# Kernel tuning notes

Hardware: AMD Instinct MI355X
Metric: run time of the kernel (lower is better)

Reference implementation:

```python
import jax, jax.numpy as jnp
import numpy as np

C = 512          # channels
G = 32           # GroupNorm groups (flax default)
H = 8            # num_heads
EPS = 1e-6       # GroupNorm epsilon (flax default)
SPATIAL = (64, 64)


def setup_inputs() -> dict:
    key = jax.random.key(0)
    k1, k2 = jax.random.split(key)
    x = jax.random.normal(k1, SPATIAL + (C,), dtype=jnp.float32)
    gn_scale = jnp.ones((C,), dtype=jnp.float32)
    gn_bias = jnp.zeros((C,), dtype=jnp.float32)
    w_qkv = jax.random.normal(k2, (C, 3 * C), dtype=jnp.float32) / np.sqrt(C)
    b_qkv = jnp.zeros((3 * C,), dtype=jnp.float32)
    return {"x": x, "gn_scale": gn_scale, "gn_bias": gn_bias,
            "w_qkv": w_qkv, "b_qkv": b_qkv}


def reference(x, gn_scale, gn_bias, w_qkv, b_qkv):
    spatial_shape = x.shape[:-1]
    T = int(np.prod(spatial_shape))
    xf = x.reshape(T, C)

    # GroupNorm over (all spatial positions, channels within group) per group
    xg = xf.reshape(T, G, C // G)
    mean = jnp.mean(xg, axis=(0, 2), keepdims=True)
    var = jnp.var(xg, axis=(0, 2), keepdims=True)
    xn = ((xg - mean) * jax.lax.rsqrt(var + EPS)).reshape(T, C)
    xn = xn * gn_scale + gn_bias

    # QKV projection; note strided split: reshape (T, 3C) -> (T, C, 3)
    qkv = (xn @ w_qkv + b_qkv).reshape(T, C, 3)
    q, k, v = qkv[..., 0], qkv[..., 1], qkv[..., 2]

    ch = C // H
    scale = 1.0 / np.sqrt(np.sqrt(ch))
    qh = (q * scale).reshape(T, H, ch)
    kh = (k * scale).reshape(T, H, ch)
    vh = v.reshape(T, H, ch)

    w = jnp.einsum('thc,shc->ths', qh, kh)      # (T, H, T) attention scores
    w = jax.nn.softmax(w, axis=-1)
    a = jnp.einsum('ths,shc->thc', w, vh)       # (T, H, ch)
    return a.reshape(spatial_shape + (C,))
```

## Files before the change

### kernel.cpp

```cpp
#include <hip/hip_runtime.h>
#include <hip/hip_bf16.h>
#include <stdint.h>

typedef __attribute__((ext_vector_type(8))) short bf16x8;
typedef __attribute__((ext_vector_type(4))) float f32x4;
typedef unsigned short u16;
typedef unsigned int u32;

constexpr int T  = 4096;
constexpr int C  = 512;
constexpr int H  = 8;
constexpr int CH = 64;
constexpr float EPS = 1e-6f;
constexpr float QKS   = 0.35355339059327378f;
constexpr float QKS_Q = 0.35355339059327378f * 1.4426950408889634f;
constexpr float M2    = 11.541560327111707f;

__device__ __forceinline__ float bf2f(u16 u) {
    union { unsigned int i; float f; } v; v.i = ((unsigned int)u) << 16; return v.f;
}
__device__ __forceinline__ u16 f2bf(float f) {
    union { float f; unsigned int i; } v; v.f = f;
    return (u16)((v.i + 0x7FFFu + ((v.i >> 16) & 1u)) >> 16);
}
__device__ __forceinline__ u32 pk2bf(float a, float b) {
    __hip_bfloat162 h = __float22bfloat162_rn(make_float2(a, b));
    u32 r; __builtin_memcpy(&r, &h, 4); return r;
}
__device__ __forceinline__ float ldin(const void* p, int i, int f32) {
    return f32 ? ((const float*)p)[i] : bf2f(((const u16*)p)[i]);
}
__device__ __forceinline__ void async16(const void* g, void* l) {
    __builtin_amdgcn_global_load_lds(
        (const __attribute__((address_space(1))) void*)g,
        (__attribute__((address_space(3))) void*)l,
        16, 0, 0);
}

__global__ void k_stats1(const void* x, float* gs, int* flag) {
    int b = blockIdx.x, tid = threadIdx.x;
    int lane = tid & 63, w = tid >> 6;
    __shared__ int cnt;
    __shared__ float red[4][32][2];
    if (tid == 0) cnt = 0;
    __syncthreads();
    const u16* u = (const u16*)x;
    int huge = 0;
    for (int i = tid; i < 1024; i += 256) {
        float a = fabsf(bf2f(u[i]));
        if (!(a < 1e4f)) huge++;
    }
    if (huge) atomicAdd(&cnt, huge);
    __syncthreads();
    int f32 = (cnt >= 8) ? 1 : 0;
    if (tid == 0) *flag = f32;
    float s1 = 0.f, s2 = 0.f;
    if (f32) {
        const float4* xp = (const float4*)x + b * 4096;
        #pragma unroll
        for (int i = 0; i < 16; i++) {
            float4 v = xp[i * 256 + tid];
            s1 += (v.x + v.y) + (v.z + v.w);
            s2 += (v.x*v.x + v.y*v.y) + (v.z*v.z + v.w*v.w);
        }
        s1 += __shfl_xor(s1, 1); s2 += __shfl_xor(s2, 1);
        s1 += __shfl_xor(s1, 2); s2 += __shfl_xor(s2, 2);
        if ((lane & 3) == 0) {
            int gl = (lane >> 2) + 16 * (w & 1);
            red[w][gl][0] = s1; red[w][gl][1] = s2;
        }
        __syncthreads();
        if (tid < 32) {
            int g = tid, w0 = (g < 16) ? 0 : 1;
            atomicAdd(&gs[g * 2],     red[w0][g][0] + red[w0 + 2][g][0]);
            atomicAdd(&gs[g * 2 + 1], red[w0][g][1] + red[w0 + 2][g][1]);
        }
    } else {
        const uint4* xp = (const uint4*)x + b * 2048;
        #pragma unroll
        for (int i = 0; i < 8; i++) {
            uint4 v = xp[i * 256 + tid];
            float f[8] = { bf2f((u16)(v.x&0xffff)), bf2f((u16)(v.x>>16)),
                           bf2f((u16)(v.y&0xffff)), bf2f((u16)(v.y>>16)),
                           bf2f((u16)(v.z&0xffff)), bf2f((u16)(v.z>>16)),
                           bf2f((u16)(v.w&0xffff)), bf2f((u16)(v.w>>16)) };
            #pragma unroll
            for (int j = 0; j < 8; j++) { s1 += f[j]; s2 += f[j]*f[j]; }
        }
        s1 += __shfl_xor(s1, 1); s2 += __shfl_xor(s2, 1);
        if ((lane & 1) == 0) { red[w][lane >> 1][0] = s1; red[w][lane >> 1][1] = s2; }
        __syncthreads();
        if (tid < 32) {
            int g = tid;
            atomicAdd(&gs[g * 2],     red[0][g][0]+red[1][g][0]+red[2][g][0]+red[3][g][0]);
            atomicAdd(&gs[g * 2 + 1], red[0][g][1]+red[1][g][1]+red[2][g][1]+red[3][g][1]);
        }
    }
}

__global__ void k_fuse(const void* x, const float* __restrict__ gs,
                       const void* gsc, const void* gbi, const void* wq,
                       u16* __restrict__ xn, u16* __restrict__ wt,
                       const int* __restrict__ flag) {
    int bx = blockIdx.x, tid = threadIdx.x;
    int f32 = *flag;
    if (bx < 1024) {
        int idx = (bx * 256 + tid) * 8;
        int c = idx & (C - 1);
        int g = c >> 4;
        float mean = gs[2 * g] * (1.0f / 65536.0f);
        float var  = gs[2 * g + 1] * (1.0f / 65536.0f) - mean * mean;
        float rstd = rsqrtf(var + EPS);
        float v[8];
        if (f32) {
            float4 x0 = *(const float4*)((const float*)x + idx);
            float4 x1 = *(const float4*)((const float*)x + idx + 4);
            v[0]=x0.x; v[1]=x0.y; v[2]=x0.z; v[3]=x0.w;
            v[4]=x1.x; v[5]=x1.y; v[6]=x1.z; v[7]=x1.w;
        } else {
            uint4 u = *(const uint4*)((const u16*)x + idx);
            v[0]=bf2f((u16)(u.x&0xffff)); v[1]=bf2f((u16)(u.x>>16));
            v[2]=bf2f((u16)(u.y&0xffff)); v[3]=bf2f((u16)(u.y>>16));
            v[4]=bf2f((u16)(u.z&0xffff)); v[5]=bf2f((u16)(u.z>>16));
            v[6]=bf2f((u16)(u.w&0xffff)); v[7]=bf2f((u16)(u.w>>16));
        }
        float r[8];
        #pragma unroll
        for (int i = 0; i < 8; i++) {
            float a = rstd * ldin(gsc, c + i, f32);
            r[i] = v[i] * a + (ldin(gbi, c + i, f32) - mean * a);
        }
        uint4 o;
        o.x = pk2bf(r[0], r[1]); o.y = pk2bf(r[2], r[3]);
        o.z = pk2bf(r[4], r[5]); o.w = pk2bf(r[6], r[7]);
        *(uint4*)(xn + idx) = o;
    } else {
        __shared__ u16 Wl[48][64];
        int b = bx - 1024;
        int k0 = (b >> 5) * 64, c0 = (b & 31) * 48;
        #pragma unroll
        for (int it = 0; it < 3; it++) {
            int u_ = it * 256 + tid;
            int r = u_ / 12, cu = u_ % 12;
            int gi = (k0 + r) * 1536 + c0 + cu * 4;
            float v0, v1, v2, v3;
            if (f32) {
                float4 t4 = *(const float4*)((const float*)wq + gi);
                v0 = t4.x; v1 = t4.y; v2 = t4.z; v3 = t4.w;
            } else {
                uint2 t2 = *(const uint2*)((const u16*)wq + gi);
                v0 = bf2f((u16)(t2.x & 0xffff)); v1 = bf2f((u16)(t2.x >> 16));
                v2 = bf2f((u16)(t2.y & 0xffff)); v3 = bf2f((u16)(t2.y >> 16));
            }
            Wl[cu*4+0][r] = f2bf(v0); Wl[cu*4+1][r] = f2bf(v1);
            Wl[cu*4+2][r] = f2bf(v2); Wl[cu*4+3][r] = f2bf(v3);
        }
        __syncthreads();
        #pragma unroll
        for (int it = 0; it < 2; it++) {
            int u_ = it * 256 + tid;
            if (u_ < 384) {
                int mrow = u_ >> 3, kc = u_ & 7;
                int j = mrow >> 4, cci = mrow & 15;
                int m = j * 512 + (c0 / 3) + cci;
                int cl = 3 * cci + j;
                uint4 val = *(const uint4*)&Wl[cl][kc * 8];
                *(uint4*)(wt + m * 512 + k0 + kc * 8) = val;
            }
        }
    }
}

__global__ __launch_bounds__(256) void k_gemm(
    const u16* __restrict__ xn, const u16* __restrict__ wt,
    const void* __restrict__ bq, const int* __restrict__ flag,
    u16* __restrict__ qh, u16* __restrict__ kh, u16* __restrict__ vt)
{
    __shared__ u16 Al[64 * 64];
    __shared__ u16 Bl[128 * 64];
    __shared__ u16 Tt[4 * 2048];
    int bx = blockIdx.x;
    int bm = bx & 63, bn = bx >> 6;
    int tid = threadIdx.x;
    int w = tid >> 6, lane = tid & 63, quad = lane >> 4, l15 = lane & 15;
    f32x4 acc[4][2] = {};
    const u16* Ag = xn + bm * 64 * 512;
    const u16* Bg = wt + bn * 128 * 512;
    for (int k0 = 0; k0 < 512; k0 += 64) {
        __syncthreads();
        #pragma unroll
        for (int i = 0; i < 2; i++) {
            int L = i * 256 + tid, row = L >> 3, cc = ((L & 7) ^ (row & 7)) * 8;
            async16(Ag + row * 512 + k0 + cc, (void*)(Al + L * 8));
        }
        #pragma unroll
        for (int i = 0; i < 4; i++) {
            int L = i * 256 + tid, row = L >> 3, cc = ((L & 7) ^ (row & 7)) * 8;
            async16(Bg + row * 512 + k0 + cc, (void*)(Bl + L * 8));
        }
        __syncthreads();
        #pragma unroll
        for (int kk = 0; kk < 2; kk++) {
            bf16x8 af[4], bfr[2];
            #pragma unroll
            for (int mi = 0; mi < 4; mi++) {
                int row = mi * 16 + l15;
                af[mi] = *(const bf16x8*)(Al + row * 64 + (((kk * 4 + quad) ^ (row & 7)) * 8));
            }
            #pragma unroll
            for (int ni = 0; ni < 2; ni++) {
                int row = w * 32 + ni * 16 + l15;
                bfr[ni] = *(const bf16x8*)(Bl + row * 64 + (((kk * 4 + quad) ^ (row & 7)) * 8));
            }
            #pragma unroll
            for (int mi = 0; mi < 4; mi++)
                #pragma unroll
                for (int ni = 0; ni < 2; ni++)
                    acc[mi][ni] = __builtin_amdgcn_mfma_f32_16x16x32_bf16(
                        af[mi], bfr[ni], acc[mi][ni], 0, 0, 0);
        }
    }
    int f32 = *flag;
    int t_base = bm * 64;
    int j = bn >> 2;
    if (j < 2) {
        u16* dst = j ? kh : qh;
        float s = j ? QKS : QKS_Q;
        #pragma unroll
        for (int ni = 0; ni < 2; ni++) {
            int n = bn * 128 + w * 32 + ni * 16 + l15;
            int r = n & 511, hh = r >> 6, cc = r & 63;
            float bias = ldin(bq, 3 * r + j, f32);
            #pragma unroll
            for (int mi = 0; mi < 4; mi++) {
                int tq = t_base + mi * 16 + quad * 4;
                #pragma unroll
                for (int rg = 0; rg < 4; rg++)
                    dst[(hh * T + tq + rg) * CH + cc] = f2bf((acc[mi][ni][rg] + bias) * s);
            }
        }
    } else {
        u16* Tw = Tt + w * 2048;
        int rbase = (bn - 8) * 128 + w * 32;
        int hh = rbase >> 6;
        #pragma unroll
        for (int ni = 0; ni < 2; ni++) {
            int r = rbase + ni * 16 + l15;
            float bias = ldin(bq, 3 * (r & 511) + 2, f32);
            int rl = ni * 16 + l15;
            #pragma unroll
            for (int mi = 0; mi < 4; mi++) {
                uint2 pv;
                pv.x = pk2bf(acc[mi][ni][0] + bias, acc[mi][ni][1] + bias);
                pv.y = pk2bf(acc[mi][ni][2] + bias, acc[mi][ni][3] + bias);
                int cs = (mi * 2 + (quad >> 1)) ^ (rl & 7);
                *(uint2*)((u32*)Tw + rl * 32 + cs * 4 + (quad & 1) * 2) = pv;
            }
        }
        int cc_hi = (w & 1) * 32;
        #pragma unroll
        for (int rr = 0; rr < 4; rr++) {
            int rl = rr * 8 + (lane >> 3);
            int g = lane & 7;
            bf16x8 val = *(const bf16x8*)(Tw + rl * 64 + ((g ^ (rl & 7)) * 8));
            *(uint4*)(vt + (hh * CH + cc_hi + rl) * T + t_base + g * 8) = *(uint4*)&val;
        }
    }
}

__global__ __launch_bounds__(256, 4) void k_attn(
    const u16* __restrict__ qh, const u16* __restrict__ kh,
    const u16* __restrict__ vt, float* __restrict__ opart, float* __restrict__ ls)
{
    __shared__ char lds[40960];
    u16* K0 = (u16*)lds;
    u16* Vl = (u16*)(lds + 16384);
    int bx = blockIdx.x;
    int h = bx >> 7, qb = (bx >> 2) & 31, ks = bx & 3;
    int t0 = qb * 128;
    int tid = threadIdx.x;
    int w = tid >> 6, lane = tid & 63, quad = lane >> 4, l15 = lane & 15;
    u16* Pw = (u16*)(lds + 24576 + w * 4096);

    const u16* Kg = kh + (h * T + ks * 1024) * CH;
    const u16* Vg = vt + h * CH * T + ks * 1024;

    bf16x8 bq[2][2];
    #pragma unroll
    for (int ni = 0; ni < 2; ni++) {
        int t = t0 + w * 32 + ni * 16 + l15;
        #pragma unroll
        for (int kk = 0; kk < 2; kk++)
            bq[ni][kk] = *(const bf16x8*)(qh + (h * T + t) * CH + kk * 32 + quad * 8);
    }

    #pragma unroll
    for (int i = 0; i < 2; i++) {
        int L = i * 256 + tid, row = L >> 3, cc = ((L & 7) ^ (row & 7)) * 8;
        async16(Kg + row * CH + cc, (void*)(K0 + L * 8));
    }

    f32x4 o[4][2] = {};
    float lsum[2] = {0.f, 0.f};

    for (int kt = 0; kt < 16; kt++) {
        u16* Kc = K0 + (kt & 1) * 4096;
        __syncthreads();
        int s0 = kt * 64;
        #pragma unroll
        for (int i = 0; i < 2; i++) {
            int L = i * 256 + tid, row = L >> 3, cc = ((L & 7) ^ (row & 7)) * 8;
            async16(Vg + row * T + s0 + cc, (void*)(Vl + L * 8));
        }
        if (kt < 15) {
            const u16* Kn = Kg + (s0 + 64) * CH;
            u16* Kd = K0 + ((kt + 1) & 1) * 4096;
            #pragma unroll
            for (int i = 0; i < 2; i++) {
                int L = i * 256 + tid, row = L >> 3, cc = ((L & 7) ^ (row & 7)) * 8;
                async16(Kn + row * CH + cc, (void*)(Kd + L * 8));
            }
        }
        f32x4 s[4][2] = {};
        #pragma unroll
        for (int kk = 0; kk < 2; kk++)
            #pragma unroll
            for (int mi = 0; mi < 4; mi++) {
                int r = mi * 16 + l15;
                bf16x8 aK = *(const bf16x8*)(Kc + r * 64 + (((kk * 4 + quad) ^ (r & 7)) * 8));
                #pragma unroll
                for (int ni = 0; ni < 2; ni++)
                    s[mi][ni] = __builtin_amdgcn_mfma_f32_16x16x32_bf16(
                        aK, bq[ni][kk], s[mi][ni], 0, 0, 0);
            }
        #pragma unroll
        for (int ni = 0; ni < 2; ni++) {
            int rl = ni * 16 + l15;
            u32* prow = (u32*)Pw + rl * 32;
            float rs = 0.f;
            #pragma unroll
            for (int mi = 0; mi < 4; mi++) {
                float e0 = exp2f(s[mi][ni][0] - M2);
                float e1 = exp2f(s[mi][ni][1] - M2);
                float e2 = exp2f(s[mi][ni][2] - M2);
                float e3 = exp2f(s[mi][ni][3] - M2);
                rs += (e0 + e1) + (e2 + e3);
                int c2 = (mi * 2 + (quad >> 1)) ^ (rl & 7);
                uint2 pv; pv.x = pk2bf(e0, e1); pv.y = pk2bf(e2, e3);
                *(uint2*)(prow + c2 * 4 + (quad & 1) * 2) = pv;
            }
            lsum[ni] += rs;
        }
        __syncthreads();
        #pragma unroll
        for (int kk = 0; kk < 2; kk++) {
            bf16x8 bp[2];
            #pragma unroll
            for (int ni = 0; ni < 2; ni++) {
                int rl = ni * 16 + l15;
                bp[ni] = *(const bf16x8*)(Pw + rl * 64 + (((kk * 4 + quad) ^ (rl & 7)) * 8));
            }
            #pragma unroll
            for (int mi = 0; mi < 4; mi++) {
                int r = mi * 16 + l15;
                bf16x8 av = *(const bf16x8*)(Vl + r * 64 + (((kk * 4 + quad) ^ (r & 7)) * 8));
                #pragma unroll
                for (int ni = 0; ni < 2; ni++)
                    o[mi][ni] = __builtin_amdgcn_mfma_f32_16x16x32_bf16(
                        av, bp[ni], o[mi][ni], 0, 0, 0);
            }
        }
    }
    #pragma unroll
    for (int ni = 0; ni < 2; ni++) {
        lsum[ni] += __shfl_xor(lsum[ni], 16);
        lsum[ni] += __shfl_xor(lsum[ni], 32);
    }
    __syncthreads();
    float* S = (float*)(lds + w * 10240);
    #pragma unroll
    for (int ni = 0; ni < 2; ni++) {
        int rl = ni * 16 + l15;
        if (quad == 0) S[2176 + rl] = lsum[ni];
        #pragma unroll
        for (int mi = 0; mi < 4; mi++)
            #pragma unroll
            for (int rg = 0; rg < 4; rg++)
                S[rl * 68 + mi * 16 + quad * 4 + rg] = o[mi][ni][rg];
    }
    int q2 = lane >> 1, dh = (lane & 1) * 32;
    int t = t0 + w * 32 + q2;
    float* od = opart + (((ks * 8 + h) * T) + t) * 64 + dh;
    #pragma unroll
    for (int i = 0; i < 8; i++)
        *(f32x4*)(od + i * 4) = *(const f32x4*)(S + q2 * 68 + dh + i * 4);
    if (lane < 32 && (lane & 1) == 0)
        ls[(ks * 8 + h) * T + t0 + w * 32 + (lane >> 1)] = S[2176 + (lane >> 1)];
    if (lane >= 32 && (lane & 1) == 0)
        ls[(ks * 8 + h) * T + t0 + w * 32 + (lane >> 1)] = S[2176 + (lane >> 1)];
}

__global__ void k_fin(const float* __restrict__ opart, const float* __restrict__ ls,
                      void* __restrict__ out, const int* __restrict__ flag) {
    int idx = (blockIdx.x * 256 + threadIdx.x) * 8;
    int d0 = idx & 63;
    int ht = idx >> 6;
    int t = ht & (T - 1), h = ht >> 12;
    float inv = 1.0f / (ls[ht] + ls[32768 + ht] + ls[65536 + ht] + ls[98304 + ht]);
    float v[8] = {};
    #pragma unroll
    for (int ks = 0; ks < 4; ks++) {
        float4 a0 = *(const float4*)(opart + ks * 2097152 + idx);
        float4 a1 = *(const float4*)(opart + ks * 2097152 + idx + 4);
        v[0] += a0.x; v[1] += a0.y; v[2] += a0.z; v[3] += a0.w;
        v[4] += a1.x; v[5] += a1.y; v[6] += a1.z; v[7] += a1.w;
    }
    #pragma unroll
    for (int i = 0; i < 8; i++) v[i] *= inv;
    int gbase = t * C + h * CH + d0;
    if (*flag) {
        *(float4*)((float*)out + gbase)     = make_float4(v[0], v[1], v[2], v[3]);
        *(float4*)((float*)out + gbase + 4) = make_float4(v[4], v[5], v[6], v[7]);
    } else {
        uint4 o;
        o.x = pk2bf(v[0], v[1]); o.y = pk2bf(v[2], v[3]);
        o.z = pk2bf(v[4], v[5]); o.w = pk2bf(v[6], v[7]);
        *(uint4*)((u16*)out + gbase) = o;
    }
}

extern "C" void kernel_launch(void* const* d_in, const int* in_sizes, int n_in,
                              void* d_out, int out_size, void* d_ws, size_t ws_size,
                              hipStream_t stream) {
    const void* x   = d_in[0];
    const void* gsc = d_in[1];
    const void* gbi = d_in[2];
    const void* wq  = d_in[3];
    const void* bq  = d_in[4];
    char* ws = (char*)d_ws;
    int*   flag = (int*)ws;
    float* gs   = (float*)(ws + 256);
    char* base = ws + 8192;
    u16* qh = (u16*)(base);
    u16* kh = (u16*)(base + 4194304);
    u16* vt = (u16*)(base + 8388608);
    u16* xn = (u16*)(base + 12582912);
    u16* wt = (u16*)(base + 16777216);
    float* opart = (float*)(base + 12582912);
    float* ls    = (float*)(base + 46137344);

    hipMemsetAsync(gs, 0, 256, stream);
    hipLaunchKernelGGL(k_stats1, dim3(128),  dim3(256), 0, stream, x, gs, flag);
    hipLaunchKernelGGL(k_fuse,   dim3(1280), dim3(256), 0, stream, x, gs, gsc, gbi, wq, xn, wt, flag);
    hipLaunchKernelGGL(k_gemm,   dim3(768),  dim3(256), 0, stream, xn, wt, bq, flag, qh, kh, vt);
    hipLaunchKernelGGL(k_attn,   dim3(1024), dim3(256), 0, stream, qh, kh, vt, opart, ls);
    hipLaunchKernelGGL(k_fin,    dim3(1024), dim3(256), 0, stream, opart, ls, d_out, flag);
}
```

Measured before the change: 175.2 us.

## Use 32x32 MFMA in attention with register P exchange; double-buffer GEMM tiles

```diff
diff --git a/kernel.cpp b/kernel.cpp
--- a/kernel.cpp
+++ b/kernel.cpp
@@ -4,6 +4,7 @@
 
 typedef __attribute__((ext_vector_type(8))) short bf16x8;
 typedef __attribute__((ext_vector_type(4))) float f32x4;
+typedef __attribute__((ext_vector_type(16))) float f32x16;
 typedef unsigned short u16;
 typedef unsigned int u32;
 
@@ -176,9 +177,9 @@
     const void* __restrict__ bq, const int* __restrict__ flag,
     u16* __restrict__ qh, u16* __restrict__ kh, u16* __restrict__ vt)
 {
-    __shared__ u16 Al[64 * 64];
-    __shared__ u16 Bl[128 * 64];
-    __shared__ u16 Tt[4 * 2048];
+    __shared__ char smem[49152];
+    u16* Al = (u16*)smem;
+    u16* Bl = (u16*)(smem + 16384);
     int bx = blockIdx.x;
     int bm = bx & 63, bn = bx >> 6;
     int tid = threadIdx.x;
@@ -186,31 +187,49 @@
     f32x4 acc[4][2] = {};
     const u16* Ag = xn + bm * 64 * 512;
     const u16* Bg = wt + bn * 128 * 512;
-    for (int k0 = 0; k0 < 512; k0 += 64) {
-        __syncthreads();
-        #pragma unroll
-        for (int i = 0; i < 2; i++) {
-            int L = i * 256 + tid, row = L >> 3, cc = ((L & 7) ^ (row & 7)) * 8;
-            async16(Ag + row * 512 + k0 + cc, (void*)(Al + L * 8));
-        }
-        #pragma unroll
-        for (int i = 0; i < 4; i++) {
-            int L = i * 256 + tid, row = L >> 3, cc = ((L & 7) ^ (row & 7)) * 8;
-            async16(Bg + row * 512 + k0 + cc, (void*)(Bl + L * 8));
-        }
-        __syncthreads();
+
+    #pragma unroll
+    for (int i = 0; i < 2; i++) {
+        int L = i * 256 + tid, row = L >> 3, cc = ((L & 7) ^ (row & 7)) * 8;
+        async16(Ag + row * 512 + cc, (void*)(Al + L * 8));
+    }
+    #pragma unroll
+    for (int i = 0; i < 4; i++) {
+        int L = i * 256 + tid, row = L >> 3, cc = ((L & 7) ^ (row & 7)) * 8;
+        async16(Bg + row * 512 + cc, (void*)(Bl + L * 8));
+    }
+
+    #pragma unroll
+    for (int ki = 0; ki < 8; ki++) {
+        __syncthreads();
+        if (ki < 7) {
+            int kn = (ki + 1) * 64;
+            int bo = ((ki + 1) & 1);
+            #pragma unroll
+            for (int i = 0; i < 2; i++) {
+                int L = i * 256 + tid, row = L >> 3, cc = ((L & 7) ^ (row & 7)) * 8;
+                async16(Ag + row * 512 + kn + cc, (void*)(Al + bo * 4096 + L * 8));
+            }
+            #pragma unroll
+            for (int i = 0; i < 4; i++) {
+                int L = i * 256 + tid, row = L >> 3, cc = ((L & 7) ^ (row & 7)) * 8;
+                async16(Bg + row * 512 + kn + cc, (void*)(Bl + bo * 8192 + L * 8));
+            }
+        }
+        const u16* Ab = Al + (ki & 1) * 4096;
+        const u16* Bb = Bl + (ki & 1) * 8192;
         #pragma unroll
         for (int kk = 0; kk < 2; kk++) {
             bf16x8 af[4], bfr[2];
             #pragma unroll
             for (int mi = 0; mi < 4; mi++) {
                 int row = mi * 16 + l15;
-                af[mi] = *(const bf16x8*)(Al + row * 64 + (((kk * 4 + quad) ^ (row & 7)) * 8));
+                af[mi] = *(const bf16x8*)(Ab + row * 64 + (((kk * 4 + quad) ^ (row & 7)) * 8));
             }
             #pragma unroll
             for (int ni = 0; ni < 2; ni++) {
                 int row = w * 32 + ni * 16 + l15;
-                bfr[ni] = *(const bf16x8*)(Bl + row * 64 + (((kk * 4 + quad) ^ (row & 7)) * 8));
+                bfr[ni] = *(const bf16x8*)(Bb + row * 64 + (((kk * 4 + quad) ^ (row & 7)) * 8));
             }
             #pragma unroll
             for (int mi = 0; mi < 4; mi++)
@@ -240,6 +259,8 @@
             }
         }
     } else {
+        __syncthreads();
+        u16* Tt = (u16*)smem;
         u16* Tw = Tt + w * 2048;
         int rbase = (bn - 8) * 128 + w * 32;
         int hh = rbase >> 6;
@@ -272,26 +293,34 @@
     const u16* __restrict__ qh, const u16* __restrict__ kh,
     const u16* __restrict__ vt, float* __restrict__ opart, float* __restrict__ ls)
 {
-    __shared__ char lds[40960];
+    __shared__ char lds[24576];
     u16* K0 = (u16*)lds;
     u16* Vl = (u16*)(lds + 16384);
     int bx = blockIdx.x;
     int h = bx >> 7, qb = (bx >> 2) & 31, ks = bx & 3;
     int t0 = qb * 128;
     int tid = threadIdx.x;
-    int w = tid >> 6, lane = tid & 63, quad = lane >> 4, l15 = lane & 15;
-    u16* Pw = (u16*)(lds + 24576 + w * 4096);
+    int w = tid >> 6, lane = tid & 63;
+    int l31 = lane & 31, hi = lane >> 5;
 
     const u16* Kg = kh + (h * T + ks * 1024) * CH;
     const u16* Vg = vt + h * CH * T + ks * 1024;
 
-    bf16x8 bq[2][2];
-    #pragma unroll
-    for (int ni = 0; ni < 2; ni++) {
-        int t = t0 + w * 32 + ni * 16 + l15;
-        #pragma unroll
-        for (int kk = 0; kk < 2; kk++)
-            bq[ni][kk] = *(const bf16x8*)(qh + (h * T + t) * CH + kk * 32 + quad * 8);
+    int off[2][4];
+    #pragma unroll
+    for (int rt = 0; rt < 2; rt++)
+        #pragma unroll
+        for (int c = 0; c < 4; c++) {
+            int row = rt * 32 + l31;
+            off[rt][c] = row * 64 + (((2 * c + hi) ^ (row & 7)) * 8);
+        }
+
+    bf16x8 bq[4];
+    {
+        const u16* qrow = qh + (h * T + t0 + w * 32 + l31) * CH;
+        #pragma unroll
+        for (int ksi = 0; ksi < 4; ksi++)
+            bq[ksi] = *(const bf16x8*)(qrow + ksi * 16 + hi * 8);
     }
 
     #pragma unroll
@@ -300,20 +329,20 @@
         async16(Kg + row * CH + cc, (void*)(K0 + L * 8));
     }
 
-    f32x4 o[4][2] = {};
-    float lsum[2] = {0.f, 0.f};
+    f32x16 o[2] = {};
+    float lsum = 0.f;
 
     for (int kt = 0; kt < 16; kt++) {
-        u16* Kc = K0 + (kt & 1) * 4096;
-        __syncthreads();
-        int s0 = kt * 64;
+        const u16* Kc = K0 + (kt & 1) * 4096;
+        __syncthreads();
+        int kbase = kt * 64;
         #pragma unroll
         for (int i = 0; i < 2; i++) {
             int L = i * 256 + tid, row = L >> 3, cc = ((L & 7) ^ (row & 7)) * 8;
-            async16(Vg + row * T + s0 + cc, (void*)(Vl + L * 8));
+            async16(Vg + row * T + kbase + cc, (void*)(Vl + L * 8));
         }
         if (kt < 15) {
-            const u16* Kn = Kg + (s0 + 64) * CH;
+            const u16* Kn = Kg + (kbase + 64) * CH;
             u16* Kd = K0 + ((kt + 1) & 1) * 4096;
             #pragma unroll
             for (int i = 0; i < 2; i++) {
@@ -321,83 +350,69 @@
                 async16(Kn + row * CH + cc, (void*)(Kd + L * 8));
             }
         }
-        f32x4 s[4][2] = {};
-        #pragma unroll
-        for (int kk = 0; kk < 2; kk++)
-            #pragma unroll
-            for (int mi = 0; mi < 4; mi++) {
-                int r = mi * 16 + l15;
-                bf16x8 aK = *(const bf16x8*)(Kc + r * 64 + (((kk * 4 + quad) ^ (r & 7)) * 8));
-                #pragma unroll
-                for (int ni = 0; ni < 2; ni++)
-                    s[mi][ni] = __builtin_amdgcn_mfma_f32_16x16x32_bf16(
-                        aK, bq[ni][kk], s[mi][ni], 0, 0, 0);
-            }
-        #pragma unroll
-        for (int ni = 0; ni < 2; ni++) {
-            int rl = ni * 16 + l15;
-            u32* prow = (u32*)Pw + rl * 32;
+        f32x16 sa[2] = {};
+        #pragma unroll
+        for (int t = 0; t < 2; t++)
+            #pragma unroll
+            for (int ksi = 0; ksi < 4; ksi++) {
+                bf16x8 aK = *(const bf16x8*)(Kc + off[t][ksi]);
+                sa[t] = __builtin_amdgcn_mfma_f32_32x32x16_bf16(aK, bq[ksi], sa[t], 0, 0, 0);
+            }
+        u32 bp[4][4];
+        #pragma unroll
+        for (int t = 0; t < 2; t++) {
+            u32 p[8], xch[8];
             float rs = 0.f;
             #pragma unroll
-            for (int mi = 0; mi < 4; mi++) {
-                float e0 = exp2f(s[mi][ni][0] - M2);
-                float e1 = exp2f(s[mi][ni][1] - M2);
-                float e2 = exp2f(s[mi][ni][2] - M2);
-                float e3 = exp2f(s[mi][ni][3] - M2);
-                rs += (e0 + e1) + (e2 + e3);
-                int c2 = (mi * 2 + (quad >> 1)) ^ (rl & 7);
-                uint2 pv; pv.x = pk2bf(e0, e1); pv.y = pk2bf(e2, e3);
-                *(uint2*)(prow + c2 * 4 + (quad & 1) * 2) = pv;
-            }
-            lsum[ni] += rs;
-        }
-        __syncthreads();
-        #pragma unroll
-        for (int kk = 0; kk < 2; kk++) {
-            bf16x8 bp[2];
-            #pragma unroll
-            for (int ni = 0; ni < 2; ni++) {
-                int rl = ni * 16 + l15;
-                bp[ni] = *(const bf16x8*)(Pw + rl * 64 + (((kk * 4 + quad) ^ (rl & 7)) * 8));
-            }
-            #pragma unroll
-            for (int mi = 0; mi < 4; mi++) {
-                int r = mi * 16 + l15;
-                bf16x8 av = *(const bf16x8*)(Vl + r * 64 + (((kk * 4 + quad) ^ (r & 7)) * 8));
-                #pragma unroll
-                for (int ni = 0; ni < 2; ni++)
-                    o[mi][ni] = __builtin_amdgcn_mfma_f32_16x16x32_bf16(
-                        av, bp[ni], o[mi][ni], 0, 0, 0);
-            }
-        }
-    }
-    #pragma unroll
-    for (int ni = 0; ni < 2; ni++) {
-        lsum[ni] += __shfl_xor(lsum[ni], 16);
-        lsum[ni] += __shfl_xor(lsum[ni], 32);
-    }
+            for (int pi = 0; pi < 8; pi++) {
+                float e0 = exp2f(sa[t][2 * pi]     - M2);
+                float e1 = exp2f(sa[t][2 * pi + 1] - M2);
+                rs += e0 + e1;
+                p[pi] = pk2bf(e0, e1);
+            }
+            lsum += rs;
+            #pragma unroll
+            for (int pi = 0; pi < 8; pi++) xch[pi] = (u32)__shfl_xor((int)p[pi], 32);
+            #pragma unroll
+            for (int k2 = 0; k2 < 2; k2++) {
+                int kst = t * 2 + k2;
+                bp[kst][0] = hi ? xch[4*k2+2] : p[4*k2+0];
+                bp[kst][1] = hi ? xch[4*k2+3] : p[4*k2+1];
+                bp[kst][2] = hi ? p[4*k2+2]   : xch[4*k2+0];
+                bp[kst][3] = hi ? p[4*k2+3]   : xch[4*k2+1];
+            }
+        }
+        __syncthreads();
+        #pragma unroll
+        for (int dt = 0; dt < 2; dt++)
+            #pragma unroll
+            for (int kst = 0; kst < 4; kst++) {
+                bf16x8 aV = *(const bf16x8*)(Vl + off[dt][kst]);
+                bf16x8 bpv;
+                __builtin_memcpy(&bpv, bp[kst], 16);
+                o[dt] = __builtin_amdgcn_mfma_f32_32x32x16_bf16(aV, bpv, o[dt], 0, 0, 0);
+            }
+    }
+    lsum += __shfl_xor(lsum, 32);
+
     __syncthreads();
-    float* S = (float*)(lds + w * 10240);
-    #pragma unroll
-    for (int ni = 0; ni < 2; ni++) {
-        int rl = ni * 16 + l15;
-        if (quad == 0) S[2176 + rl] = lsum[ni];
-        #pragma unroll
-        for (int mi = 0; mi < 4; mi++)
-            #pragma unroll
-            for (int rg = 0; rg < 4; rg++)
-                S[rl * 68 + mi * 16 + quad * 4 + rg] = o[mi][ni][rg];
-    }
-    int q2 = lane >> 1, dh = (lane & 1) * 32;
-    int t = t0 + w * 32 + q2;
-    float* od = opart + (((ks * 8 + h) * T) + t) * 64 + dh;
-    #pragma unroll
-    for (int i = 0; i < 8; i++)
-        *(f32x4*)(od + i * 4) = *(const f32x4*)(S + q2 * 68 + dh + i * 4);
-    if (lane < 32 && (lane & 1) == 0)
-        ls[(ks * 8 + h) * T + t0 + w * 32 + (lane >> 1)] = S[2176 + (lane >> 1)];
-    if (lane >= 32 && (lane & 1) == 0)
-        ls[(ks * 8 + h) * T + t0 + w * 32 + (lane >> 1)] = S[2176 + (lane >> 1)];
+    float* Sw = (float*)(lds + w * 6144);
+    int qg = t0 + w * 32;
+    int q2 = lane >> 1, half = lane & 1;
+    #pragma unroll
+    for (int dt = 0; dt < 2; dt++) {
+        #pragma unroll
+        for (int reg = 0; reg < 16; reg++) {
+            int dl = (reg & 3) + 8 * (reg >> 2) + 4 * hi;
+            Sw[l31 * 33 + dl] = o[dt][reg];
+        }
+        const float* src = Sw + q2 * 33 + half * 16;
+        float* dst = opart + ((ks * 8 + h) * T + qg + q2) * 64 + dt * 32 + half * 16;
+        #pragma unroll
+        for (int i = 0; i < 4; i++)
+            *(f32x4*)(dst + i * 4) = *(const f32x4*)(src + i * 4);
+    }
+    if (hi == 0) ls[(ks * 8 + h) * T + qg + l31] = lsum;
 }
 
 __global__ void k_fin(const float* __restrict__ opart, const float* __restrict__ ls,
```

After: 174.5 us. About the same (-0.4%).
